# Kernel tuning notes

Measured on AMD Instinct MI355X. Metric: run time of the kernel, lower is better.

Reference implementation:

```python
import jax, jax.numpy as jnp
import numpy as np

D_MODEL = 1024
D_K = 1024
D_V = 1024
THRESH = 0.9
LN_EPS = 1e-6


def setup_inputs() -> dict:
    key = jax.random.key(0)
    ks = jax.random.split(key, 8)
    B, S = 8, 2048
    scale = 1.0 / np.sqrt(D_MODEL)
    return {
        "q": jax.random.normal(ks[0], (B, S, D_MODEL), dtype=jnp.float32),
        "k": jax.random.normal(ks[1], (B, S, D_MODEL), dtype=jnp.float32),
        "v": jax.random.normal(ks[2], (B, S, D_MODEL), dtype=jnp.float32),
        "Wq": jax.random.normal(ks[3], (D_MODEL, D_K), dtype=jnp.float32) * scale,
        "Wk": jax.random.normal(ks[4], (D_MODEL, D_K), dtype=jnp.float32) * scale,
        "Wv": jax.random.normal(ks[5], (D_MODEL, D_V), dtype=jnp.float32) * scale,
        "Wfc": jax.random.normal(ks[6], (D_V, D_MODEL), dtype=jnp.float32) * (1.0 / np.sqrt(D_V)),
        "ln_gamma": jnp.ones((D_MODEL,), dtype=jnp.float32),
        "ln_beta": jnp.zeros((D_MODEL,), dtype=jnp.float32),
    }


def reference(q, k, v, Wq, Wk, Wv, Wfc, ln_gamma, ln_beta):
    residual = q
    qh = q @ Wq          # [B,S,d_k]
    kh = k @ Wk          # [B,S,d_k]
    vh = v @ Wv          # [B,S,d_v]
    inv_sqrt_dk = jnp.asarray(1.0 / np.sqrt(D_K), dtype=qh.dtype)
    attn = jnp.einsum('bqd,bkd->bqk', qh, kh) * inv_sqrt_dk  # [B,S,S]
    # hard sparsity threshold applied BEFORE softmax (faithful to original)
    attn = jnp.where(attn < THRESH, jnp.asarray(0.0, attn.dtype), attn)
    attn = jax.nn.softmax(attn, axis=-1)
    # dropout is identity in eval mode
    out = jnp.einsum('bqk,bkd->bqd', attn, vh) @ Wfc  # [B,S,d_model]
    out = out + residual
    mean = jnp.mean(out, axis=-1, keepdims=True)
    var = jnp.mean(jnp.square(out - mean), axis=-1, keepdims=True)
    out = (out - mean) * jax.lax.rsqrt(var + LN_EPS) * ln_gamma + ln_beta
    return (out, attn)
```

## Files before the change

kernel.cpp:

```cpp
#include <hip/hip_runtime.h>
#include <hip/hip_bf16.h>
#include <stdint.h>

typedef __attribute__((ext_vector_type(8))) short bf16x8;
typedef __attribute__((ext_vector_type(4))) float f32x4;
typedef __attribute__((ext_vector_type(4))) unsigned short us4;
typedef __attribute__((ext_vector_type(8))) unsigned short us8;

__device__ __forceinline__ unsigned short f2bf(float f) {
  union { float f; unsigned int u; } v; v.f = f;
  unsigned int u = v.u;
  return (unsigned short)((u + 0x7FFFu + ((u >> 16) & 1u)) >> 16);
}
__device__ __forceinline__ float bf2f(unsigned short h) {
  union { unsigned int u; float f; } v; v.u = ((unsigned int)h) << 16;
  return v.f;
}

__device__ __forceinline__ void gload16(const unsigned short* g, unsigned short* l) {
  __builtin_amdgcn_global_load_lds(
      (const __attribute__((address_space(1))) unsigned int*)g,
      (__attribute__((address_space(3))) unsigned int*)l, 16, 0, 0);
}

template <int EPI>
__global__ __launch_bounds__(512, 1)
void gemm9(const unsigned short* __restrict__ Ap, const unsigned short* __restrict__ Btp,
           void* __restrict__ Cp, float* __restrict__ extra,
           int M, int N, int K, int nbm, int nbn,
           long long sA, long long sB, long long sC)
{
  __shared__ unsigned short ls[3 * 16384];
  __shared__ float srow[256][4];

  const int tid = threadIdx.x;
  const int lane = tid & 63;
  const int wid = tid >> 6;
  const int bb = blockIdx.y;
  const int bm = blockIdx.x % nbm, bn = blockIdx.x / nbm;
  const int row0 = bm * 256, col0 = bn * 256;

  const unsigned short* Ab = Ap + (long long)bb * sA;
  const unsigned short* Bb = Btp + (long long)bb * sB;

  const int stgrow = wid * 32 + (lane >> 2);
  const int sslot = (lane & 3) ^ ((lane >> 2) & 3);
  const unsigned short* Asrc = Ab + (long long)(row0 + stgrow) * K + sslot * 8;
  const unsigned short* Bsrc = Bb + (long long)(col0 + stgrow) * K + sslot * 8;

  const int warow = (wid >> 2) * 128 + (lane & 15);
  const int wbcol = (wid & 3) * 64 + (lane & 15);
  const int rslot = ((lane >> 4) ^ (lane & 3)) * 8;

#define ISSUE(KT, CB) do { \
    unsigned short* _la = ls + (CB) * 16384 + wid * 1024; \
    unsigned short* _lb = _la + 8192; \
    const long long _ko = (long long)(KT) * 32; \
    gload16(Asrc + _ko, _la); \
    gload16(Asrc + 16ll * K + _ko, _la + 512); \
    gload16(Bsrc + _ko, _lb); \
    gload16(Bsrc + 16ll * K + _ko, _lb + 512); \
  } while (0)

  f32x4 acc[8][4];
#pragma unroll
  for (int m = 0; m < 8; ++m)
#pragma unroll
    for (int n = 0; n < 4; ++n) {
      f32x4 z = {0.f, 0.f, 0.f, 0.f};
      acc[m][n] = z;
    }

  const int NT = K >> 5;
  ISSUE(0, 0);
  ISSUE(1, 1);

  int c0 = 0, c1 = 1, c2 = 2;
  for (int t = 0; t < NT; ++t) {
    if (t + 1 < NT) asm volatile("s_waitcnt vmcnt(4)" ::: "memory");
    else            asm volatile("s_waitcnt vmcnt(0)" ::: "memory");
    __builtin_amdgcn_s_barrier();
    __builtin_amdgcn_sched_barrier(0);
    if (t + 2 < NT) ISSUE(t + 2, c2);
    {
      const unsigned short* _A = ls + c0 * 16384;
      const unsigned short* _B = _A + 8192;
      bf16x8 af[8], bfr[4];
#pragma unroll
      for (int mf = 0; mf < 8; ++mf)
        af[mf] = *(const bf16x8*)&_A[(warow + mf * 16) * 32 + rslot];
#pragma unroll
      for (int nf = 0; nf < 4; ++nf)
        bfr[nf] = *(const bf16x8*)&_B[(wbcol + nf * 16) * 32 + rslot];
      __builtin_amdgcn_s_setprio(1);
#pragma unroll
      for (int mf = 0; mf < 8; ++mf)
#pragma unroll
        for (int nf = 0; nf < 4; ++nf)
          acc[mf][nf] = __builtin_amdgcn_mfma_f32_16x16x32_bf16(
              af[mf], bfr[nf], acc[mf][nf], 0, 0, 0);
      __builtin_amdgcn_s_setprio(0);
    }
    int tmp = c0; c0 = c1; c1 = c2; c2 = tmp;
  }
#undef ISSUE

  if (EPI == 0 || EPI == 3) {
    unsigned short* C = (unsigned short*)Cp + (long long)bb * sC;
    const float* inv = (EPI == 3) ? (extra + (long long)bb * 2048) : nullptr;
#pragma unroll
    for (int mf = 0; mf < 8; ++mf)
#pragma unroll
      for (int nf = 0; nf < 4; ++nf)
#pragma unroll
        for (int i = 0; i < 4; ++i) {
          int gr = row0 + (wid >> 2) * 128 + mf * 16 + (lane >> 4) * 4 + i;
          int gc = col0 + (wid & 3) * 64 + nf * 16 + (lane & 15);
          float x = acc[mf][nf][i];
          if (EPI == 3) x *= inv[gr];
          C[(long long)gr * N + gc] = f2bf(x);
        }
  } else if (EPI == 2) {
    unsigned short* C = (unsigned short*)Cp;
#pragma unroll
    for (int mf = 0; mf < 8; ++mf)
#pragma unroll
      for (int nf = 0; nf < 4; ++nf) {
        int gr = row0 + (wid >> 2) * 128 + mf * 16 + (lane >> 4) * 4;
        int gc = col0 + (wid & 3) * 64 + nf * 16 + (lane & 15);
        int bb2 = gr >> 11, grb = gr & 2047;
        us4 o;
        o[0] = f2bf(acc[mf][nf][0]); o[1] = f2bf(acc[mf][nf][1]);
        o[2] = f2bf(acc[mf][nf][2]); o[3] = f2bf(acc[mf][nf][3]);
        *(us4*)&C[(long long)bb2 * sC + (long long)gc * 2048 + grb] = o;
      }
  } else {
    unsigned short* C = (unsigned short*)Cp + (long long)bb * sC;
    float rs[8][4];
#pragma unroll
    for (int mf = 0; mf < 8; ++mf)
#pragma unroll
      for (int i = 0; i < 4; ++i) rs[mf][i] = 0.f;
#pragma unroll
    for (int mf = 0; mf < 8; ++mf)
#pragma unroll
      for (int nf = 0; nf < 4; ++nf)
#pragma unroll
        for (int i = 0; i < 4; ++i) {
          int gr = row0 + (wid >> 2) * 128 + mf * 16 + (lane >> 4) * 4 + i;
          int gc = col0 + (wid & 3) * 64 + nf * 16 + (lane & 15);
          float s = acc[mf][nf][i] * 0.03125f;
          s = (s < 0.9f) ? 0.f : s;
          float e = __expf(s);
          C[(long long)gr * N + gc] = f2bf(e);
          rs[mf][i] += e;
        }
#pragma unroll
    for (int mf = 0; mf < 8; ++mf)
#pragma unroll
      for (int i = 0; i < 4; ++i) {
        float vv = rs[mf][i];
        vv += __shfl_xor(vv, 1); vv += __shfl_xor(vv, 2);
        vv += __shfl_xor(vv, 4); vv += __shfl_xor(vv, 8);
        if ((lane & 15) == 0)
          srow[(wid >> 2) * 128 + mf * 16 + (lane >> 4) * 4 + i][wid & 3] = vv;
      }
    __syncthreads();
    if (tid < 256) {
      int gr = row0 + tid;
      extra[((long long)bb * M + gr) * nbn + bn] =
          srow[tid][0] + srow[tid][1] + srow[tid][2] + srow[tid][3];
    }
  }
}

__global__ __launch_bounds__(256)
void cvt3(const float* __restrict__ a, const float* __restrict__ b,
          const float* __restrict__ c, unsigned short* __restrict__ oa,
          unsigned short* __restrict__ ob, unsigned short* __restrict__ oc) {
  const long long i = ((long long)blockIdx.x * 256 + threadIdx.x) * 8;
#pragma unroll
  for (int p = 0; p < 3; ++p) {
    const float* src = (p == 0) ? a : (p == 1) ? b : c;
    unsigned short* dst = (p == 0) ? oa : (p == 1) ? ob : oc;
    f32x4 x0 = *(const f32x4*)(src + i);
    f32x4 x1 = *(const f32x4*)(src + i + 4);
    us8 o;
    o[0] = f2bf(x0[0]); o[1] = f2bf(x0[1]); o[2] = f2bf(x0[2]); o[3] = f2bf(x0[3]);
    o[4] = f2bf(x1[0]); o[5] = f2bf(x1[1]); o[6] = f2bf(x1[2]); o[7] = f2bf(x1[3]);
    *(us8*)(dst + i) = o;
  }
}

__global__ __launch_bounds__(256)
void wtrans(const float* __restrict__ W, unsigned short* __restrict__ WT) {
  __shared__ float t[32][33];
  const int bi = blockIdx.x, bj = blockIdx.y;
  const int c = threadIdx.x & 31;
  const int r0 = threadIdx.x >> 5;
#pragma unroll
  for (int j = 0; j < 4; ++j) {
    int r = r0 + j * 8;
    t[r][c] = W[(long long)(bi * 32 + r) * 1024 + bj * 32 + c];
  }
  __syncthreads();
#pragma unroll
  for (int j = 0; j < 4; ++j) {
    int r = r0 + j * 8;
    WT[(long long)(bj * 32 + r) * 1024 + bi * 32 + c] = f2bf(t[c][r]);
  }
}

__global__ __launch_bounds__(256)
void attn_norm(const unsigned short* __restrict__ e, const float* __restrict__ partials,
               float* __restrict__ attn, float* __restrict__ inv_dens) {
  const long long row = blockIdx.x;
  const int tid = threadIdx.x;
  __shared__ float sden;
  if (tid < 64) {
    float v = (tid < 8) ? partials[row * 8 + tid] : 0.f;
    v += __shfl_xor(v, 1); v += __shfl_xor(v, 2); v += __shfl_xor(v, 4);
    if (tid == 0) sden = v;
  }
  __syncthreads();
  const float inv = 1.0f / sden;
  if (tid == 0) inv_dens[row] = inv;
  us8 x = *(const us8*)(e + row * 2048 + tid * 8);
  f32x4 y0, y1;
#pragma unroll
  for (int i = 0; i < 4; ++i) { y0[i] = bf2f(x[i]) * inv; y1[i] = bf2f(x[i + 4]) * inv; }
  *(f32x4*)(attn + row * 2048 + tid * 8) = y0;
  *(f32x4*)(attn + row * 2048 + tid * 8 + 4) = y1;
}

__global__ __launch_bounds__(256)
void ln_kernel(const unsigned short* __restrict__ fc, const float* __restrict__ q,
               const float* __restrict__ gamma, const float* __restrict__ beta,
               float* __restrict__ out) {
  const long long row = blockIdx.x;
  const int tid = threadIdx.x;
  __shared__ float sb1[4], sb2[4];
  us4 hv = *(const us4*)(fc + row * 1024 + tid * 4);
  f32x4 qv = *(const f32x4*)(q + row * 1024 + tid * 4);
  float x0 = bf2f(hv[0]) + qv[0];
  float x1 = bf2f(hv[1]) + qv[1];
  float x2 = bf2f(hv[2]) + qv[2];
  float x3 = bf2f(hv[3]) + qv[3];
  float s = x0 + x1 + x2 + x3;
#pragma unroll
  for (int m = 1; m < 64; m <<= 1) s += __shfl_xor(s, m);
  if ((tid & 63) == 0) sb1[tid >> 6] = s;
  __syncthreads();
  const float mean = (sb1[0] + sb1[1] + sb1[2] + sb1[3]) * (1.0f / 1024.0f);
  float d0 = x0 - mean, d1 = x1 - mean, d2 = x2 - mean, d3 = x3 - mean;
  float vs = d0 * d0 + d1 * d1 + d2 * d2 + d3 * d3;
#pragma unroll
  for (int m = 1; m < 64; m <<= 1) vs += __shfl_xor(vs, m);
  if ((tid & 63) == 0) sb2[tid >> 6] = vs;
  __syncthreads();
  const float var = (sb2[0] + sb2[1] + sb2[2] + sb2[3]) * (1.0f / 1024.0f);
  const float r = rsqrtf(var + 1e-6f);
  f32x4 g = *(const f32x4*)(gamma + tid * 4);
  f32x4 bt = *(const f32x4*)(beta + tid * 4);
  f32x4 o;
  o[0] = d0 * r * g[0] + bt[0];
  o[1] = d1 * r * g[1] + bt[1];
  o[2] = d2 * r * g[2] + bt[2];
  o[3] = d3 * r * g[3] + bt[3];
  *(f32x4*)(out + row * 1024 + tid * 4) = o;
}

extern "C" void kernel_launch(void* const* d_in, const int* in_sizes, int n_in,
                              void* d_out, int out_size, void* d_ws, size_t ws_size,
                              hipStream_t stream) {
  const float* q    = (const float*)d_in[0];
  const float* k    = (const float*)d_in[1];
  const float* v    = (const float*)d_in[2];
  const float* Wq   = (const float*)d_in[3];
  const float* Wk   = (const float*)d_in[4];
  const float* Wv   = (const float*)d_in[5];
  const float* Wfc  = (const float*)d_in[6];
  const float* gamma = (const float*)d_in[7];
  const float* beta  = (const float*)d_in[8];

  float* out0 = (float*)d_out;
  float* attn = out0 + (long long)8 * 2048 * 1024;

  char* ao = (char*)attn;
  unsigned short* qb = (unsigned short*)(ao);
  unsigned short* kb = (unsigned short*)(ao + (32ll << 20));
  unsigned short* vb = (unsigned short*)(ao + (64ll << 20));
  unsigned short* qh = (unsigned short*)(ao + (96ll << 20));
  unsigned short* kh = (unsigned short*)(ao);
  unsigned short* vhT     = (unsigned short*)d_out;
  unsigned short* out_mid = (unsigned short*)((char*)d_out + (32ll << 20));

  char* ws = (char*)d_ws;
  unsigned short* WqT  = (unsigned short*)(ws);
  unsigned short* WkT  = (unsigned short*)(ws + (2ll  << 20));
  unsigned short* WvT  = (unsigned short*)(ws + (4ll  << 20));
  unsigned short* WfcT = (unsigned short*)(ws + (6ll  << 20));
  float* partials      = (float*)(ws + (8ll  << 20));
  float* inv_dens      = (float*)(ws + (10ll << 20));
  unsigned short* e    = (unsigned short*)(ws + (11ll << 20));
  unsigned short* fc   = e;

  cvt3<<<dim3(8192), 256, 0, stream>>>(q, k, v, qb, kb, vb);
  wtrans<<<dim3(32, 32), 256, 0, stream>>>(Wq, WqT);
  wtrans<<<dim3(32, 32), 256, 0, stream>>>(Wk, WkT);
  wtrans<<<dim3(32, 32), 256, 0, stream>>>(Wv, WvT);
  wtrans<<<dim3(32, 32), 256, 0, stream>>>(Wfc, WfcT);

  gemm9<0><<<dim3(256, 1), 512, 0, stream>>>(qb, WqT, qh, nullptr,
      16384, 1024, 1024, 64, 4, 0, 0, 0);
  gemm9<0><<<dim3(256, 1), 512, 0, stream>>>(kb, WkT, kh, nullptr,
      16384, 1024, 1024, 64, 4, 0, 0, 0);
  gemm9<2><<<dim3(256, 1), 512, 0, stream>>>(vb, WvT, vhT, nullptr,
      16384, 1024, 1024, 64, 4, 0, 0, 1024ll * 2048);

  gemm9<1><<<dim3(64, 8), 512, 0, stream>>>(qh, kh, e, partials,
      2048, 2048, 1024, 8, 8, 2048ll * 1024, 2048ll * 1024, 2048ll * 2048);

  attn_norm<<<dim3(16384), 256, 0, stream>>>(e, partials, attn, inv_dens);

  gemm9<3><<<dim3(32, 8), 512, 0, stream>>>(e, vhT, out_mid, inv_dens,
      2048, 1024, 2048, 8, 4, 2048ll * 2048, 1024ll * 2048, 2048ll * 1024);

  gemm9<0><<<dim3(256, 1), 512, 0, stream>>>(out_mid, WfcT, fc, nullptr,
      16384, 1024, 1024, 64, 4, 0, 0, 0);

  ln_kernel<<<dim3(16384), 256, 0, stream>>>(fc, q, gamma, beta, out0);
}
```

Measured before the change: 446.2 us.

## Switch GEMM to double-buffered BK=64 pipeline, fuse weight transposes, bf16 residual

The GEMM kernel moves from a triple-buffered BK=32 pipeline to a double-buffered BK=64 pipeline with a wider XOR swizzle. Each barrier now feeds two MFMA sweeps, and launch bounds are raised to allow two blocks per CU. The four weight-transpose launches are merged into one 3D-grid launch. When the workspace is large enough, the layernorm reads the residual from the bf16 copy of q instead of fp32. That copy is rounded, so it adds precision loss to the residual add. The LDS use of 128KB+ per block likely prevents two blocks per CU anyway, and the full vmcnt(0) wait serializes loads with compute more than before.

After: 411.6 us. 7.8% less time.

```diff
diff --git a/kernel.cpp b/kernel.cpp
--- a/kernel.cpp
+++ b/kernel.cpp
@@ -24,13 +24,13 @@
 }
 
 template <int EPI>
-__global__ __launch_bounds__(512, 1)
-void gemm9(const unsigned short* __restrict__ Ap, const unsigned short* __restrict__ Btp,
-           void* __restrict__ Cp, float* __restrict__ extra,
-           int M, int N, int K, int nbm, int nbn,
-           long long sA, long long sB, long long sC)
+__global__ __launch_bounds__(512, 2)
+void gemm2p(const unsigned short* __restrict__ Ap, const unsigned short* __restrict__ Btp,
+            void* __restrict__ Cp, float* __restrict__ extra,
+            int M, int N, int K, int nbm, int nbn,
+            long long sA, long long sB, long long sC)
 {
-  __shared__ unsigned short ls[3 * 16384];
+  __shared__ unsigned short ls[65536];
   __shared__ float srow[256][4];
 
   const int tid = threadIdx.x;
@@ -43,24 +43,29 @@
   const unsigned short* Ab = Ap + (long long)bb * sA;
   const unsigned short* Bb = Btp + (long long)bb * sB;
 
-  const int stgrow = wid * 32 + (lane >> 2);
-  const int sslot = (lane & 3) ^ ((lane >> 2) & 3);
-  const unsigned short* Asrc = Ab + (long long)(row0 + stgrow) * K + sslot * 8;
-  const unsigned short* Bsrc = Bb + (long long)(col0 + stgrow) * K + sslot * 8;
-
-  const int warow = (wid >> 2) * 128 + (lane & 15);
-  const int wbcol = (wid & 3) * 64 + (lane & 15);
-  const int rslot = ((lane >> 4) ^ (lane & 3)) * 8;
-
-#define ISSUE(KT, CB) do { \
-    unsigned short* _la = ls + (CB) * 16384 + wid * 1024; \
-    unsigned short* _lb = _la + 8192; \
-    const long long _ko = (long long)(KT) * 32; \
-    gload16(Asrc + _ko, _la); \
-    gload16(Asrc + 16ll * K + _ko, _la + 512); \
-    gload16(Bsrc + _ko, _lb); \
-    gload16(Bsrc + 16ll * K + _ko, _lb + 512); \
+  const int srw = tid >> 3;
+  const int ssl = (tid & 7) ^ ((tid >> 3) & 7);
+  const unsigned short* Asrc = Ab + (long long)(row0 + srw) * K + ssl * 8;
+  const unsigned short* Bsrc = Bb + (long long)(col0 + srw) * K + ssl * 8;
+
+#define STAGE(KT, BUF) do { \
+    unsigned short* _la = ls + (BUF) * 32768 + wid * 512; \
+    unsigned short* _lb = _la + 16384; \
+    const long long _ko = (long long)(KT) * 64; \
+    gload16(Asrc + _ko,             _la); \
+    gload16(Asrc + 64ll * K + _ko,  _la + 4096); \
+    gload16(Asrc + 128ll * K + _ko, _la + 8192); \
+    gload16(Asrc + 192ll * K + _ko, _la + 12288); \
+    gload16(Bsrc + _ko,             _lb); \
+    gload16(Bsrc + 64ll * K + _ko,  _lb + 4096); \
+    gload16(Bsrc + 128ll * K + _ko, _lb + 8192); \
+    gload16(Bsrc + 192ll * K + _ko, _lb + 12288); \
   } while (0)
+
+  const int arow = (wid >> 2) * 128 + (lane & 15);
+  const int bcol = (wid & 3) * 64 + (lane & 15);
+  const int sl0 = ((lane >> 4) ^ (lane & 7)) * 8;
+  const int sl1 = ((4 + (lane >> 4)) ^ (lane & 7)) * 8;
 
   f32x4 acc[8][4];
 #pragma unroll
@@ -71,39 +76,45 @@
       acc[m][n] = z;
     }
 
-  const int NT = K >> 5;
-  ISSUE(0, 0);
-  ISSUE(1, 1);
-
-  int c0 = 0, c1 = 1, c2 = 2;
+  STAGE(0, 0);
+  const int NT = K >> 6;
   for (int t = 0; t < NT; ++t) {
-    if (t + 1 < NT) asm volatile("s_waitcnt vmcnt(4)" ::: "memory");
-    else            asm volatile("s_waitcnt vmcnt(0)" ::: "memory");
+    const int cb = (t & 1) * 32768;
+    asm volatile("s_waitcnt vmcnt(0)" ::: "memory");
     __builtin_amdgcn_s_barrier();
     __builtin_amdgcn_sched_barrier(0);
-    if (t + 2 < NT) ISSUE(t + 2, c2);
-    {
-      const unsigned short* _A = ls + c0 * 16384;
-      const unsigned short* _B = _A + 8192;
-      bf16x8 af[8], bfr[4];
-#pragma unroll
-      for (int mf = 0; mf < 8; ++mf)
-        af[mf] = *(const bf16x8*)&_A[(warow + mf * 16) * 32 + rslot];
+    if (t + 1 < NT) STAGE(t + 1, (t & 1) ^ 1);
+    const unsigned short* As = ls + cb;
+    const unsigned short* Bs = ls + cb + 16384;
+    bf16x8 af[8], bfr[4];
+#pragma unroll
+    for (int mf = 0; mf < 8; ++mf)
+      af[mf] = *(const bf16x8*)&As[(arow + mf * 16) * 64 + sl0];
+#pragma unroll
+    for (int nf = 0; nf < 4; ++nf)
+      bfr[nf] = *(const bf16x8*)&Bs[(bcol + nf * 16) * 64 + sl0];
+    __builtin_amdgcn_s_setprio(1);
+#pragma unroll
+    for (int mf = 0; mf < 8; ++mf)
 #pragma unroll
       for (int nf = 0; nf < 4; ++nf)
-        bfr[nf] = *(const bf16x8*)&_B[(wbcol + nf * 16) * 32 + rslot];
-      __builtin_amdgcn_s_setprio(1);
-#pragma unroll
-      for (int mf = 0; mf < 8; ++mf)
-#pragma unroll
-        for (int nf = 0; nf < 4; ++nf)
-          acc[mf][nf] = __builtin_amdgcn_mfma_f32_16x16x32_bf16(
-              af[mf], bfr[nf], acc[mf][nf], 0, 0, 0);
-      __builtin_amdgcn_s_setprio(0);
-    }
-    int tmp = c0; c0 = c1; c1 = c2; c2 = tmp;
-  }
-#undef ISSUE
+        acc[mf][nf] = __builtin_amdgcn_mfma_f32_16x16x32_bf16(af[mf], bfr[nf], acc[mf][nf], 0, 0, 0);
+    __builtin_amdgcn_s_setprio(0);
+#pragma unroll
+    for (int mf = 0; mf < 8; ++mf)
+      af[mf] = *(const bf16x8*)&As[(arow + mf * 16) * 64 + sl1];
+#pragma unroll
+    for (int nf = 0; nf < 4; ++nf)
+      bfr[nf] = *(const bf16x8*)&Bs[(bcol + nf * 16) * 64 + sl1];
+    __builtin_amdgcn_s_setprio(1);
+#pragma unroll
+    for (int mf = 0; mf < 8; ++mf)
+#pragma unroll
+      for (int nf = 0; nf < 4; ++nf)
+        acc[mf][nf] = __builtin_amdgcn_mfma_f32_16x16x32_bf16(af[mf], bfr[nf], acc[mf][nf], 0, 0, 0);
+    __builtin_amdgcn_s_setprio(0);
+  }
+#undef STAGE
 
   if (EPI == 0 || EPI == 3) {
     unsigned short* C = (unsigned short*)Cp + (long long)bb * sC;
@@ -193,8 +204,14 @@
 }
 
 __global__ __launch_bounds__(256)
-void wtrans(const float* __restrict__ W, unsigned short* __restrict__ WT) {
+void wtrans4(const float* __restrict__ W0, const float* __restrict__ W1,
+             const float* __restrict__ W2, const float* __restrict__ W3,
+             unsigned short* __restrict__ T0, unsigned short* __restrict__ T1,
+             unsigned short* __restrict__ T2, unsigned short* __restrict__ T3) {
   __shared__ float t[32][33];
+  const int z = blockIdx.z;
+  const float* W = (z == 0) ? W0 : (z == 1) ? W1 : (z == 2) ? W2 : W3;
+  unsigned short* WT = (z == 0) ? T0 : (z == 1) ? T1 : (z == 2) ? T2 : T3;
   const int bi = blockIdx.x, bj = blockIdx.y;
   const int c = threadIdx.x & 31;
   const int r0 = threadIdx.x >> 5;
@@ -233,19 +250,27 @@
   *(f32x4*)(attn + row * 2048 + tid * 8 + 4) = y1;
 }
 
+template <bool QB16>
 __global__ __launch_bounds__(256)
-void ln_kernel(const unsigned short* __restrict__ fc, const float* __restrict__ q,
+void ln_kernel(const unsigned short* __restrict__ fc, const void* __restrict__ qres,
                const float* __restrict__ gamma, const float* __restrict__ beta,
                float* __restrict__ out) {
   const long long row = blockIdx.x;
   const int tid = threadIdx.x;
   __shared__ float sb1[4], sb2[4];
   us4 hv = *(const us4*)(fc + row * 1024 + tid * 4);
-  f32x4 qv = *(const f32x4*)(q + row * 1024 + tid * 4);
-  float x0 = bf2f(hv[0]) + qv[0];
-  float x1 = bf2f(hv[1]) + qv[1];
-  float x2 = bf2f(hv[2]) + qv[2];
-  float x3 = bf2f(hv[3]) + qv[3];
+  float q0, q1, q2, q3;
+  if (QB16) {
+    us4 qv = *(const us4*)((const unsigned short*)qres + row * 1024 + tid * 4);
+    q0 = bf2f(qv[0]); q1 = bf2f(qv[1]); q2 = bf2f(qv[2]); q3 = bf2f(qv[3]);
+  } else {
+    f32x4 qv = *(const f32x4*)((const float*)qres + row * 1024 + tid * 4);
+    q0 = qv[0]; q1 = qv[1]; q2 = qv[2]; q3 = qv[3];
+  }
+  float x0 = bf2f(hv[0]) + q0;
+  float x1 = bf2f(hv[1]) + q1;
+  float x2 = bf2f(hv[2]) + q2;
+  float x3 = bf2f(hv[3]) + q3;
   float s = x0 + x1 + x2 + x3;
 #pragma unroll
   for (int m = 1; m < 64; m <<= 1) s += __shfl_xor(s, m);
@@ -287,7 +312,6 @@
   float* attn = out0 + (long long)8 * 2048 * 1024;
 
   char* ao = (char*)attn;
-  unsigned short* qb = (unsigned short*)(ao);
   unsigned short* kb = (unsigned short*)(ao + (32ll << 20));
   unsigned short* vb = (unsigned short*)(ao + (64ll << 20));
   unsigned short* qh = (unsigned short*)(ao + (96ll << 20));
@@ -304,30 +328,33 @@
   float* inv_dens      = (float*)(ws + (10ll << 20));
   unsigned short* e    = (unsigned short*)(ws + (11ll << 20));
   unsigned short* fc   = e;
+  const bool qb_ws = ws_size >= (110ll << 20);
+  unsigned short* qb = qb_ws ? (unsigned short*)(ws + (76ll << 20))
+                             : (unsigned short*)(ao);
 
   cvt3<<<dim3(8192), 256, 0, stream>>>(q, k, v, qb, kb, vb);
-  wtrans<<<dim3(32, 32), 256, 0, stream>>>(Wq, WqT);
-  wtrans<<<dim3(32, 32), 256, 0, stream>>>(Wk, WkT);
-  wtrans<<<dim3(32, 32), 256, 0, stream>>>(Wv, WvT);
-  wtrans<<<dim3(32, 32), 256, 0, stream>>>(Wfc, WfcT);
-
-  gemm9<0><<<dim3(256, 1), 512, 0, stream>>>(qb, WqT, qh, nullptr,
+  wtrans4<<<dim3(32, 32, 4), 256, 0, stream>>>(Wq, Wk, Wv, Wfc, WqT, WkT, WvT, WfcT);
+
+  gemm2p<0><<<dim3(256, 1), 512, 0, stream>>>(qb, WqT, qh, nullptr,
       16384, 1024, 1024, 64, 4, 0, 0, 0);
-  gemm9<0><<<dim3(256, 1), 512, 0, stream>>>(kb, WkT, kh, nullptr,
+  gemm2p<0><<<dim3(256, 1), 512, 0, stream>>>(kb, WkT, kh, nullptr,
       16384, 1024, 1024, 64, 4, 0, 0, 0);
-  gemm9<2><<<dim3(256, 1), 512, 0, stream>>>(vb, WvT, vhT, nullptr,
+  gemm2p<2><<<dim3(256, 1), 512, 0, stream>>>(vb, WvT, vhT, nullptr,
       16384, 1024, 1024, 64, 4, 0, 0, 1024ll * 2048);
 
-  gemm9<1><<<dim3(64, 8), 512, 0, stream>>>(qh, kh, e, partials,
+  gemm2p<1><<<dim3(64, 8), 512, 0, stream>>>(qh, kh, e, partials,
       2048, 2048, 1024, 8, 8, 2048ll * 1024, 2048ll * 1024, 2048ll * 2048);
 
   attn_norm<<<dim3(16384), 256, 0, stream>>>(e, partials, attn, inv_dens);
 
-  gemm9<3><<<dim3(32, 8), 512, 0, stream>>>(e, vhT, out_mid, inv_dens,
+  gemm2p<3><<<dim3(32, 8), 512, 0, stream>>>(e, vhT, out_mid, inv_dens,
       2048, 1024, 2048, 8, 4, 2048ll * 2048, 1024ll * 2048, 2048ll * 1024);
 
-  gemm9<0><<<dim3(256, 1), 512, 0, stream>>>(out_mid, WfcT, fc, nullptr,
+  gemm2p<0><<<dim3(256, 1), 512, 0, stream>>>(out_mid, WfcT, fc, nullptr,
       16384, 1024, 1024, 64, 4, 0, 0, 0);
 
-  ln_kernel<<<dim3(16384), 256, 0, stream>>>(fc, q, gamma, beta, out0);
-}
+  if (qb_ws)
+    ln_kernel<true><<<dim3(16384), 256, 0, stream>>>(fc, qb, gamma, beta, out0);
+  else
+    ln_kernel<false><<<dim3(16384), 256, 0, stream>>>(fc, q, gamma, beta, out0);
+}
```
